# Optimization experiments

Hardware: AMD Instinct MI355X
Metric: run time of the kernel (lower is better)

Reference implementation:

```python
import jax, jax.numpy as jnp
import numpy as np

EPS = 1e-5
NUM_HEADS = 8
KEY_DIM = 16
D = 64  # attn_ratio * key_dim


def conv1x1_bn(x, w, g, b, m, v):
    # x: (B, Cin, H, W), w: (Cout, Cin); eval-mode BatchNorm over channel dim
    y = jnp.einsum('bchw,oc->bohw', x, w)
    scale = (g * jax.lax.rsqrt(v + EPS))[None, :, None, None]
    shift = (b - g * m * jax.lax.rsqrt(v + EPS))[None, :, None, None]
    return y * scale + shift


def setup_inputs() -> dict:
    key = jax.random.key(0)
    ks = jax.random.split(key, 22)
    dim, nh_kd, dh = 384, 128, 512
    f = jax.random.normal
    u = jax.random.uniform
    return {
        'x': f(ks[0], (2, dim, 56, 56), jnp.float32),
        'wq': f(ks[1], (nh_kd, dim), jnp.float32) * 0.05,
        'qg': u(ks[2], (nh_kd,), jnp.float32), 'qb': f(ks[3], (nh_kd,)) * 0.1,
        'qm': f(ks[4], (nh_kd,)) * 0.1, 'qv': u(ks[5], (nh_kd,)) + 0.5,
        'wk': f(ks[6], (nh_kd, dim), jnp.float32) * 0.05,
        'kg': u(ks[7], (nh_kd,), jnp.float32), 'kb': f(ks[8], (nh_kd,)) * 0.1,
        'km': f(ks[9], (nh_kd,)) * 0.1, 'kvv': u(ks[10], (nh_kd,)) + 0.5,
        'wv': f(ks[11], (dh, dim), jnp.float32) * 0.05,
        'vg': u(ks[12], (dh,), jnp.float32), 'vb': f(ks[13], (dh,)) * 0.1,
        'vm': f(ks[14], (dh,)) * 0.1, 'vvv': u(ks[15], (dh,)) + 0.5,
        'wp': f(ks[16], (dim, dh), jnp.float32) * 0.05,
        'pg': u(ks[17], (dim,), jnp.float32), 'pb': f(ks[18], (dim,)) * 0.1,
        'pm': f(ks[19], (dim,)) * 0.1, 'pvv': u(ks[20], (dim,)) + 0.5,
    }


def reference(x, wq, qg, qb, qm, qv, wk, kg, kb, km, kvv,
              wv, vg, vb, vm, vvv, wp, pg, pb, pm, pvv):
    B, C, H, W = x.shape
    N = H * W
    h, kd, d = NUM_HEADS, KEY_DIM, D
    # (B, h, N, kd)
    qq = conv1x1_bn(x, wq, qg, qb, qm, qv).reshape(B, h, kd, N).transpose(0, 1, 3, 2)
    # (B, h, kd, N)
    kk = conv1x1_bn(x, wk, kg, kb, km, kvv).reshape(B, h, kd, N)
    # (B, h, N, d)
    vv = conv1x1_bn(x, wv, vg, vb, vm, vvv).reshape(B, h, d, N).transpose(0, 1, 3, 2)
    # NOTE: original forward does NOT apply self.scale
    attn = jax.nn.softmax(jnp.matmul(qq, kk), axis=-1)  # (B, h, N, N)
    xx = jnp.matmul(attn, vv)                            # (B, h, N, d)
    xx = xx.transpose(0, 1, 3, 2).reshape(B, h * d, H, W)
    xx = jax.nn.relu(xx)
    return conv1x1_bn(xx, wp, pg, pb, pm, pvv)
```

## Files before the change

kernel.cpp:

```cpp
#include <hip/hip_runtime.h>
#include <hip/hip_bf16.h>

#define B_   2
#define CIN  384
#define NPIX 3136
#define NH   8
#define KD   16
#define DHEAD 64
#define NHKD 128
#define DHD  512
#define EPSW 1e-5f

typedef __attribute__((ext_vector_type(8))) short vshort8;
typedef __attribute__((ext_vector_type(4))) short vshort4;
typedef __attribute__((ext_vector_type(4))) float vfloat4;

static __device__ __forceinline__ float bf2f(short s) {
    unsigned int u = ((unsigned int)(unsigned short)s) << 16;
    return __builtin_bit_cast(float, u);
}
static __device__ __forceinline__ short f2bf(float f) {
    unsigned int u = __builtin_bit_cast(unsigned int, f);
    unsigned int lsb = (u >> 16) & 1u;
    u += 0x7fffu + lsb;
    return (short)(u >> 16);
}
static __device__ __forceinline__ float pget(const void* p, int i, int f32) {
    return f32 ? ((const float*)p)[i] : bf2f(((const short*)p)[i]);
}

__global__ void detect_dtype(const unsigned short* __restrict__ x, int* __restrict__ flag) {
    if (threadIdx.x == 0 && blockIdx.x == 0) {
        int big = 0;
        for (int i = 0; i < 512; i += 2) {
            int e = (x[i] >> 7) & 0xFF;
            if (e >= 0xC0) big++;
        }
        *flag = (big >= 8) ? 1 : 0;
    }
}

__global__ __launch_bounds__(256) void convert_weights(
    const void* __restrict__ wq, const void* __restrict__ wk,
    const void* __restrict__ wv, const void* __restrict__ wp,
    short* __restrict__ wB, const int* __restrict__ flag)
{
    int f32 = *flag;
    int i = blockIdx.x * 256 + threadIdx.x;
    const void* src; int j;
    if (i < 49152)       { src = wq; j = i; }
    else if (i < 98304)  { src = wk; j = i - 49152; }
    else if (i < 294912) { src = wv; j = i - 98304; }
    else                 { src = wp; j = i - 294912; }
    wB[i] = f32 ? f2bf(((const float*)src)[j]) : ((const short*)src)[j];
}

__global__ __launch_bounds__(256) void transpose_k(const void* __restrict__ x,
                                                   short* __restrict__ xT,
                                                   const int* __restrict__ flag) {
    __shared__ short tile[32][33];
    int f32 = *flag;
    int b = blockIdx.z, n0 = blockIdx.x * 32, c0 = blockIdx.y * 32;
    int t = threadIdx.x;
    int r = t >> 3, q4 = (t & 7) * 4;
    size_t off = ((size_t)b * CIN + c0 + r) * NPIX + n0 + q4;
    if (f32) {
        float4 v = *(const float4*)((const float*)x + off);
        tile[r][q4 + 0] = f2bf(v.x);
        tile[r][q4 + 1] = f2bf(v.y);
        tile[r][q4 + 2] = f2bf(v.z);
        tile[r][q4 + 3] = f2bf(v.w);
    } else {
        vshort4 v = *(const vshort4*)((const short*)x + off);
#pragma unroll
        for (int i = 0; i < 4; i++) tile[r][q4 + i] = v[i];
    }
    __syncthreads();
    vshort4 o;
#pragma unroll
    for (int i = 0; i < 4; i++) o[i] = tile[q4 + i][r];
    *(vshort4*)(xT + ((size_t)b * NPIX + n0 + r) * CIN + c0 + q4) = o;
}

__global__ __launch_bounds__(256) void gemm_bt_bn(
    const short* __restrict__ A, long sAb,
    const short* __restrict__ Bt, long sBb,
    void* __restrict__ C, long sCb,
    const void* __restrict__ g, const void* __restrict__ bb,
    const void* __restrict__ mn, const void* __restrict__ vr,
    int Ma, int Nb, int K, int bnPerRow, int finalOut,
    const int* __restrict__ flag)
{
    __shared__ __attribute__((aligned(16))) short Al[64 * 72];
    __shared__ __attribute__((aligned(16))) short Bl[64 * 72];
    int f32 = *flag;
    int b = blockIdx.z;
    const short* Ab = A + (size_t)b * sAb;
    const short* Bb = Bt + (size_t)b * sBb;
    size_t cbase = (size_t)b * sCb;
    int m0 = blockIdx.x * 64, n0 = blockIdx.y * 64;
    int t = threadIdx.x, lane = t & 63, w = t >> 6, m = lane & 15, quad = lane >> 4;
    int srow = t >> 2, scol = (t & 3) * 16;
    const short* ag = Ab + (size_t)(m0 + srow) * K + scol;
    const short* bg = Bb + (size_t)(n0 + srow) * K + scol;
    vfloat4 acc[4];
#pragma unroll
    for (int i = 0; i < 4; i++) acc[i] = (vfloat4){0.f, 0.f, 0.f, 0.f};

    for (int k0 = 0; k0 < K; k0 += 64) {
        vshort8 a0 = *(const vshort8*)(ag + k0);
        vshort8 a1 = *(const vshort8*)(ag + k0 + 8);
        vshort8 b0 = *(const vshort8*)(bg + k0);
        vshort8 b1 = *(const vshort8*)(bg + k0 + 8);
        __syncthreads();
        *(vshort8*)&Al[srow * 72 + scol] = a0;
        *(vshort8*)&Al[srow * 72 + scol + 8] = a1;
        *(vshort8*)&Bl[srow * 72 + scol] = b0;
        *(vshort8*)&Bl[srow * 72 + scol + 8] = b1;
        __syncthreads();
#pragma unroll
        for (int kk = 0; kk < 2; kk++) {
            vshort8 af = *(const vshort8*)&Al[(w * 16 + m) * 72 + kk * 32 + quad * 8];
#pragma unroll
            for (int nc = 0; nc < 4; nc++) {
                vshort8 bf = *(const vshort8*)&Bl[(nc * 16 + m) * 72 + kk * 32 + quad * 8];
                acc[nc] = __builtin_amdgcn_mfma_f32_16x16x32_bf16(af, bf, acc[nc], 0, 0, 0);
            }
        }
    }

#pragma unroll
    for (int nc = 0; nc < 4; nc++) {
#pragma unroll
        for (int r = 0; r < 4; r++) {
            int row = m0 + w * 16 + quad * 4 + r;
            int col = n0 + nc * 16 + m;
            int ch = bnPerRow ? row : col;
            float iv = rsqrtf(pget(vr, ch, f32) + EPSW);
            float sc = pget(g, ch, f32) * iv;
            float sh = pget(bb, ch, f32) - pget(mn, ch, f32) * sc;
            float val = sc * acc[nc][r] + sh;
            size_t idx = cbase + (size_t)row * Nb + col;
            if (finalOut && f32) ((float*)C)[idx] = val;
            else                 ((short*)C)[idx] = f2bf(val);
        }
    }
}

__global__ __launch_bounds__(256) void attn_kernel(
    const short* __restrict__ Qt, const short* __restrict__ Kt,
    const short* __restrict__ V, short* __restrict__ xx)
{
    __shared__ __attribute__((aligned(16))) short Kl[64 * 40];
    __shared__ __attribute__((aligned(16))) short Vl[64 * 72];
    __shared__ __attribute__((aligned(16))) short Pl[64 * 72];
    __shared__ float Ls[64];
    int bh = blockIdx.y, b = bh >> 3, h = bh & 7;
    int q0 = blockIdx.x * 64;
    int t = threadIdx.x, lane = t & 63, w = t >> 6, m = lane & 15, quad = lane >> 4;

    {
        int key = t >> 2;
        int z = 16 + (t & 3) * 4;
        *(vshort4*)&Kl[key * 40 + z] = (vshort4){0, 0, 0, 0};
    }

    int q = q0 + w * 16 + m;
    vshort8 aq;
    if (quad < 2) {
        aq = *(const vshort8*)(Qt + ((size_t)b * NPIX + q) * NHKD + h * KD + quad * 8);
    } else {
        aq = (vshort8){0, 0, 0, 0, 0, 0, 0, 0};
    }

    vfloat4 o[4];
#pragma unroll
    for (int i = 0; i < 4; i++) o[i] = (vfloat4){0.f, 0.f, 0.f, 0.f};
    float Lr = 0.f;

    int skey = t >> 2, skd = (t & 3) * 4;
    const short* kgp = Kt + ((size_t)b * NPIX) * NHKD + h * KD + skd;
    int vrow = t >> 2, vcol = (t & 3) * 16;
    const short* vgp = V + ((size_t)(b * DHD) + h * DHEAD + vrow) * NPIX + vcol;
    const vfloat4 zero4 = (vfloat4){0.f, 0.f, 0.f, 0.f};

    for (int k0 = 0; k0 < NPIX; k0 += 64) {
        vshort4 kstg = *(const vshort4*)(kgp + (size_t)(k0 + skey) * NHKD);
        vshort8 v0 = *(const vshort8*)(vgp + k0);
        vshort8 v1 = *(const vshort8*)(vgp + k0 + 8);
        __syncthreads();
        *(vshort4*)&Kl[skey * 40 + skd] = kstg;
        *(vshort8*)&Vl[vrow * 72 + vcol] = v0;
        *(vshort8*)&Vl[vrow * 72 + vcol + 8] = v1;
        __syncthreads();

        vfloat4 s[4];
#pragma unroll
        for (int c = 0; c < 4; c++) {
            vshort8 ak = *(const vshort8*)&Kl[(c * 16 + m) * 40 + quad * 8];
            s[c] = __builtin_amdgcn_mfma_f32_16x16x32_bf16(ak, aq, zero4, 0, 0, 0);
        }

        short* pw = &Pl[(w * 16 + m) * 72];
#pragma unroll
        for (int c = 0; c < 4; c++) {
            vshort4 pv;
#pragma unroll
            for (int r = 0; r < 4; r++) {
                float p = __expf(s[c][r]);
                Lr += p;
                pv[r] = f2bf(p);
            }
            *(vshort4*)&pw[c * 16 + quad * 4] = pv;
        }

#pragma unroll
        for (int kc = 0; kc < 2; kc++) {
            vshort8 ap = *(const vshort8*)&Pl[(w * 16 + m) * 72 + kc * 32 + quad * 8];
#pragma unroll
            for (int dc = 0; dc < 4; dc++) {
                vshort8 bv = *(const vshort8*)&Vl[(dc * 16 + m) * 72 + kc * 32 + quad * 8];
                o[dc] = __builtin_amdgcn_mfma_f32_16x16x32_bf16(ap, bv, o[dc], 0, 0, 0);
            }
        }
    }

    Lr += __shfl_xor(Lr, 16);
    Lr += __shfl_xor(Lr, 32);
    Ls[w * 16 + m] = Lr;
    __syncthreads();

#pragma unroll
    for (int r = 0; r < 4; r++) {
        float inv = 1.0f / Ls[w * 16 + quad * 4 + r];
        int qrow = q0 + w * 16 + quad * 4 + r;
        size_t base = ((size_t)b * NPIX + qrow) * DHD + h * DHEAD + m;
#pragma unroll
        for (int dc = 0; dc < 4; dc++) {
            float val = o[dc][r] * inv;
            val = fmaxf(val, 0.0f);
            xx[base + dc * 16] = f2bf(val);
        }
    }
}

extern "C" void kernel_launch(void* const* d_in, const int* in_sizes, int n_in,
                              void* d_out, int out_size, void* d_ws, size_t ws_size,
                              hipStream_t stream) {
    const void* x  = d_in[0];
    const void* wq = d_in[1];
    const void* qg = d_in[2];  const void* qb = d_in[3];
    const void* qm = d_in[4];  const void* qv = d_in[5];
    const void* wk = d_in[6];
    const void* kg = d_in[7];  const void* kb = d_in[8];
    const void* km = d_in[9];  const void* kv = d_in[10];
    const void* wv = d_in[11];
    const void* vg = d_in[12]; const void* vb = d_in[13];
    const void* vm = d_in[14]; const void* vv = d_in[15];
    const void* wp = d_in[16];
    const void* pg = d_in[17]; const void* pb = d_in[18];
    const void* pm = d_in[19]; const void* pv = d_in[20];

    short* xT  = (short*)d_ws;
    short* wB  = xT + (size_t)B_ * NPIX * CIN;
    short* wqB = wB;
    short* wkB = wB + 49152;
    short* wvB = wB + 98304;
    short* wpB = wB + 294912;
    short* Qt  = wB + 491520;
    short* Kt  = Qt + (size_t)B_ * NPIX * NHKD;
    short* Vb  = Kt + (size_t)B_ * NPIX * NHKD;
    short* xx  = Vb + (size_t)B_ * DHD * NPIX;
    int* flag  = (int*)(xx + (size_t)B_ * NPIX * DHD);

    detect_dtype<<<1, 64, 0, stream>>>((const unsigned short*)x, flag);
    convert_weights<<<491520 / 256, 256, 0, stream>>>(wq, wk, wv, wp, wB, flag);
    transpose_k<<<dim3(NPIX / 32, CIN / 32, B_), 256, 0, stream>>>(x, xT, flag);

    gemm_bt_bn<<<dim3(NPIX / 64, NHKD / 64, B_), 256, 0, stream>>>(
        xT, (long)NPIX * CIN, wqB, 0, Qt, (long)NPIX * NHKD,
        qg, qb, qm, qv, NPIX, NHKD, CIN, 0, 0, flag);
    gemm_bt_bn<<<dim3(NPIX / 64, NHKD / 64, B_), 256, 0, stream>>>(
        xT, (long)NPIX * CIN, wkB, 0, Kt, (long)NPIX * NHKD,
        kg, kb, km, kv, NPIX, NHKD, CIN, 0, 0, flag);
    gemm_bt_bn<<<dim3(DHD / 64, NPIX / 64, B_), 256, 0, stream>>>(
        wvB, 0, xT, (long)NPIX * CIN, Vb, (long)DHD * NPIX,
        vg, vb, vm, vv, DHD, NPIX, CIN, 1, 0, flag);

    attn_kernel<<<dim3(NPIX / 64, B_ * NH), 256, 0, stream>>>(Qt, Kt, Vb, xx);

    gemm_bt_bn<<<dim3(CIN / 64, NPIX / 64, B_), 256, 0, stream>>>(
        wpB, 0, xx, (long)NPIX * DHD, d_out, (long)CIN * NPIX,
        pg, pb, pm, pv, CIN, NPIX, DHD, 1, 1, flag);
}
```

Before: 236.3 us.

## Double-buffer attention loads, fuse Q/K GEMMs, precompute BN affine, MFMA row sums

New measurement: 214.0 us. 1.1x faster.

```diff
diff --git a/kernel.cpp b/kernel.cpp
--- a/kernel.cpp
+++ b/kernel.cpp
@@ -8,6 +8,7 @@
 #define KD   16
 #define DHEAD 64
 #define NHKD 128
+#define QKW  256
 #define DHD  512
 #define EPSW 1e-5f
 
@@ -30,29 +31,54 @@
 }
 
 __global__ void detect_dtype(const unsigned short* __restrict__ x, int* __restrict__ flag) {
-    if (threadIdx.x == 0 && blockIdx.x == 0) {
-        int big = 0;
-        for (int i = 0; i < 512; i += 2) {
-            int e = (x[i] >> 7) & 0xFF;
-            if (e >= 0xC0) big++;
-        }
-        *flag = (big >= 8) ? 1 : 0;
-    }
-}
-
-__global__ __launch_bounds__(256) void convert_weights(
+    int lane = threadIdx.x & 63;
+    int cnt = 0;
+#pragma unroll
+    for (int j = 0; j < 8; j++) {
+        int e = (x[(lane * 8 + j) * 2] >> 7) & 0xFF;
+        cnt += (e >= 0xC0);
+    }
+    cnt += __shfl_xor(cnt, 1);
+    cnt += __shfl_xor(cnt, 2);
+    cnt += __shfl_xor(cnt, 4);
+    cnt += __shfl_xor(cnt, 8);
+    cnt += __shfl_xor(cnt, 16);
+    cnt += __shfl_xor(cnt, 32);
+    if (threadIdx.x == 0) *flag = (cnt >= 16) ? 1 : 0;
+}
+
+__global__ __launch_bounds__(256) void convert_and_bn(
     const void* __restrict__ wq, const void* __restrict__ wk,
     const void* __restrict__ wv, const void* __restrict__ wp,
-    short* __restrict__ wB, const int* __restrict__ flag)
+    short* __restrict__ wB,
+    const void* qg, const void* qb, const void* qm, const void* qv,
+    const void* kg, const void* kb, const void* km, const void* kv,
+    const void* vg, const void* vb, const void* vm, const void* vv,
+    const void* pg, const void* pb, const void* pm, const void* pv,
+    float* __restrict__ scA, float* __restrict__ shA,
+    const int* __restrict__ flag)
 {
     int f32 = *flag;
     int i = blockIdx.x * 256 + threadIdx.x;
-    const void* src; int j;
-    if (i < 49152)       { src = wq; j = i; }
-    else if (i < 98304)  { src = wk; j = i - 49152; }
-    else if (i < 294912) { src = wv; j = i - 98304; }
-    else                 { src = wp; j = i - 294912; }
-    wB[i] = f32 ? f2bf(((const float*)src)[j]) : ((const short*)src)[j];
+    {
+        const void* src; int j;
+        if (i < 49152)       { src = wq; j = i; }
+        else if (i < 98304)  { src = wk; j = i - 49152; }
+        else if (i < 294912) { src = wv; j = i - 98304; }
+        else                 { src = wp; j = i - 294912; }
+        wB[i] = f32 ? f2bf(((const float*)src)[j]) : ((const short*)src)[j];
+    }
+    if (i < 1152) {
+        const void *g, *bb, *mn, *vr; int j;
+        if (i < 128)      { g = qg; bb = qb; mn = qm; vr = qv; j = i; }
+        else if (i < 256) { g = kg; bb = kb; mn = km; vr = kv; j = i - 128; }
+        else if (i < 768) { g = vg; bb = vb; mn = vm; vr = vv; j = i - 256; }
+        else              { g = pg; bb = pb; mn = pm; vr = pv; j = i - 768; }
+        float iv = rsqrtf(pget(vr, j, f32) + EPSW);
+        float s = pget(g, j, f32) * iv;
+        scA[i] = s;
+        shA[i] = pget(bb, j, f32) - pget(mn, j, f32) * s;
+    }
 }
 
 __global__ __launch_bounds__(256) void transpose_k(const void* __restrict__ x,
@@ -86,14 +112,13 @@
     const short* __restrict__ A, long sAb,
     const short* __restrict__ Bt, long sBb,
     void* __restrict__ C, long sCb,
-    const void* __restrict__ g, const void* __restrict__ bb,
-    const void* __restrict__ mn, const void* __restrict__ vr,
-    int Ma, int Nb, int K, int bnPerRow, int finalOut,
+    const float* __restrict__ sc, const float* __restrict__ sh,
+    int Nb, int K, int bnPerRow, int finalOut,
     const int* __restrict__ flag)
 {
     __shared__ __attribute__((aligned(16))) short Al[64 * 72];
     __shared__ __attribute__((aligned(16))) short Bl[64 * 72];
-    int f32 = *flag;
+    int f32 = finalOut ? *flag : 0;
     int b = blockIdx.z;
     const short* Ab = A + (size_t)b * sAb;
     const short* Bb = Bt + (size_t)b * sBb;
@@ -131,15 +156,15 @@
 
 #pragma unroll
     for (int nc = 0; nc < 4; nc++) {
+        int col = n0 + nc * 16 + m;
+        float scc = bnPerRow ? 0.f : sc[col];
+        float shc = bnPerRow ? 0.f : sh[col];
 #pragma unroll
         for (int r = 0; r < 4; r++) {
             int row = m0 + w * 16 + quad * 4 + r;
-            int col = n0 + nc * 16 + m;
-            int ch = bnPerRow ? row : col;
-            float iv = rsqrtf(pget(vr, ch, f32) + EPSW);
-            float sc = pget(g, ch, f32) * iv;
-            float sh = pget(bb, ch, f32) - pget(mn, ch, f32) * sc;
-            float val = sc * acc[nc][r] + sh;
+            float s2 = bnPerRow ? sc[row] : scc;
+            float h2 = bnPerRow ? sh[row] : shc;
+            float val = s2 * acc[nc][r] + h2;
             size_t idx = cbase + (size_t)row * Nb + col;
             if (finalOut && f32) ((float*)C)[idx] = val;
             else                 ((short*)C)[idx] = f2bf(val);
@@ -148,13 +173,12 @@
 }
 
 __global__ __launch_bounds__(256) void attn_kernel(
-    const short* __restrict__ Qt, const short* __restrict__ Kt,
-    const short* __restrict__ V, short* __restrict__ xx)
+    const short* __restrict__ QKt, const short* __restrict__ V,
+    short* __restrict__ xx)
 {
-    __shared__ __attribute__((aligned(16))) short Kl[64 * 40];
-    __shared__ __attribute__((aligned(16))) short Vl[64 * 72];
+    __shared__ __attribute__((aligned(16))) short Kl[2][64 * 40];
+    __shared__ __attribute__((aligned(16))) short Vl[2][64 * 72];
     __shared__ __attribute__((aligned(16))) short Pl[64 * 72];
-    __shared__ float Ls[64];
     int bh = blockIdx.y, b = bh >> 3, h = bh & 7;
     int q0 = blockIdx.x * 64;
     int t = threadIdx.x, lane = t & 63, w = t >> 6, m = lane & 15, quad = lane >> 4;
@@ -162,42 +186,56 @@
     {
         int key = t >> 2;
         int z = 16 + (t & 3) * 4;
-        *(vshort4*)&Kl[key * 40 + z] = (vshort4){0, 0, 0, 0};
+        *(vshort4*)&Kl[0][key * 40 + z] = (vshort4){0, 0, 0, 0};
+        *(vshort4*)&Kl[1][key * 40 + z] = (vshort4){0, 0, 0, 0};
     }
 
     int q = q0 + w * 16 + m;
     vshort8 aq;
     if (quad < 2) {
-        aq = *(const vshort8*)(Qt + ((size_t)b * NPIX + q) * NHKD + h * KD + quad * 8);
+        aq = *(const vshort8*)(QKt + ((size_t)b * NPIX + q) * QKW + h * KD + quad * 8);
     } else {
         aq = (vshort8){0, 0, 0, 0, 0, 0, 0, 0};
     }
 
-    vfloat4 o[4];
+    vfloat4 o[4], o4;
 #pragma unroll
     for (int i = 0; i < 4; i++) o[i] = (vfloat4){0.f, 0.f, 0.f, 0.f};
-    float Lr = 0.f;
+    o4 = (vfloat4){0.f, 0.f, 0.f, 0.f};
 
     int skey = t >> 2, skd = (t & 3) * 4;
-    const short* kgp = Kt + ((size_t)b * NPIX) * NHKD + h * KD + skd;
+    const short* kgp = QKt + (size_t)b * NPIX * QKW + NHKD + h * KD + skd;
     int vrow = t >> 2, vcol = (t & 3) * 16;
     const short* vgp = V + ((size_t)(b * DHD) + h * DHEAD + vrow) * NPIX + vcol;
     const vfloat4 zero4 = (vfloat4){0.f, 0.f, 0.f, 0.f};
-
-    for (int k0 = 0; k0 < NPIX; k0 += 64) {
-        vshort4 kstg = *(const vshort4*)(kgp + (size_t)(k0 + skey) * NHKD);
-        vshort8 v0 = *(const vshort8*)(vgp + k0);
-        vshort8 v1 = *(const vshort8*)(vgp + k0 + 8);
-        __syncthreads();
-        *(vshort4*)&Kl[skey * 40 + skd] = kstg;
-        *(vshort8*)&Vl[vrow * 72 + vcol] = v0;
-        *(vshort8*)&Vl[vrow * 72 + vcol + 8] = v1;
-        __syncthreads();
+    const short one_bf = (short)0x3F80;
+    const vshort8 ones = {one_bf, one_bf, one_bf, one_bf, one_bf, one_bf, one_bf, one_bf};
+
+    {
+        vshort4 kstg = *(const vshort4*)(kgp + (size_t)skey * QKW);
+        vshort8 v0 = *(const vshort8*)(vgp);
+        vshort8 v1 = *(const vshort8*)(vgp + 8);
+        *(vshort4*)&Kl[0][skey * 40 + skd] = kstg;
+        *(vshort8*)&Vl[0][vrow * 72 + vcol] = v0;
+        *(vshort8*)&Vl[0][vrow * 72 + vcol + 8] = v1;
+    }
+    __syncthreads();
+
+    for (int it = 0; it < NPIX / 64; ++it) {
+        int cur = it & 1, nxt = cur ^ 1;
+        int k0 = it * 64;
+        int more = (it + 1) < (NPIX / 64);
+        vshort4 kstg; vshort8 v0, v1;
+        if (more) {
+            kstg = *(const vshort4*)(kgp + (size_t)(k0 + 64 + skey) * QKW);
+            v0 = *(const vshort8*)(vgp + k0 + 64);
+            v1 = *(const vshort8*)(vgp + k0 + 72);
+        }
 
         vfloat4 s[4];
 #pragma unroll
         for (int c = 0; c < 4; c++) {
-            vshort8 ak = *(const vshort8*)&Kl[(c * 16 + m) * 40 + quad * 8];
+            vshort8 ak = *(const vshort8*)&Kl[cur][(c * 16 + m) * 40 + quad * 8];
             s[c] = __builtin_amdgcn_mfma_f32_16x16x32_bf16(ak, aq, zero4, 0, 0, 0);
         }
 
@@ -208,8 +246,7 @@
 #pragma unroll
             for (int r = 0; r < 4; r++) {
                 float p = __expf(s[c][r]);
-                Lr += p;
-                pv[r] = f2bf(p);
+                pv[r] = (short)(__builtin_bit_cast(unsigned int, p) >> 16);
             }
             *(vshort4*)&pw[c * 16 + quad * 4] = pv;
         }
@@ -219,20 +256,23 @@
             vshort8 ap = *(const vshort8*)&Pl[(w * 16 + m) * 72 + kc * 32 + quad * 8];
 #pragma unroll
             for (int dc = 0; dc < 4; dc++) {
-                vshort8 bv = *(const vshort8*)&Vl[(dc * 16 + m) * 72 + kc * 32 + quad * 8];
+                vshort8 bv = *(const vshort8*)&Vl[cur][(dc * 16 + m) * 72 + kc * 32 + quad * 8];
                 o[dc] = __builtin_amdgcn_mfma_f32_16x16x32_bf16(ap, bv, o[dc], 0, 0, 0);
             }
-        }
-    }
-
-    Lr += __shfl_xor(Lr, 16);
-    Lr += __shfl_xor(Lr, 32);
-    Ls[w * 16 + m] = Lr;
-    __syncthreads();
+            o4 = __builtin_amdgcn_mfma_f32_16x16x32_bf16(ap, ones, o4, 0, 0, 0);
+        }
+
+        if (more) {
+            *(vshort4*)&Kl[nxt][skey * 40 + skd] = kstg;
+            *(vshort8*)&Vl[nxt][vrow * 72 + vcol] = v0;
+            *(vshort8*)&Vl[nxt][vrow * 72 + vcol + 8] = v1;
+        }
+        __syncthreads();
+    }
 
 #pragma unroll
     for (int r = 0; r < 4; r++) {
-        float inv = 1.0f / Ls[w * 16 + quad * 4 + r];
+        float inv = 1.0f / o4[r];
         int qrow = q0 + w * 16 + quad * 4 + r;
         size_t base = ((size_t)b * NPIX + qrow) * DHD + h * DHEAD + m;
 #pragma unroll
@@ -263,33 +303,33 @@
 
     short* xT  = (short*)d_ws;
     short* wB  = xT + (size_t)B_ * NPIX * CIN;
-    short* wqB = wB;
-    short* wkB = wB + 49152;
-    short* wvB = wB + 98304;
-    short* wpB = wB + 294912;
-    short* Qt  = wB + 491520;
-    short* Kt  = Qt + (size_t)B_ * NPIX * NHKD;
-    short* Vb  = Kt + (size_t)B_ * NPIX * NHKD;
+    short* wqkB = wB;
+    short* wvB  = wB + 98304;
+    short* wpB  = wB + 294912;
+    short* QKt = wB + 491520;
+    short* Vb  = QKt + (size_t)B_ * NPIX * QKW;
     short* xx  = Vb + (size_t)B_ * DHD * NPIX;
-    int* flag  = (int*)(xx + (size_t)B_ * NPIX * DHD);
+    float* scA = (float*)(xx + (size_t)B_ * NPIX * DHD);
+    float* shA = scA + 1152;
+    int* flag  = (int*)(shA + 1152);
 
     detect_dtype<<<1, 64, 0, stream>>>((const unsigned short*)x, flag);
-    convert_weights<<<491520 / 256, 256, 0, stream>>>(wq, wk, wv, wp, wB, flag);
+    convert_and_bn<<<491520 / 256, 256, 0, stream>>>(
+        wq, wk, wv, wp, wB,
+        qg, qb, qm, qv, kg, kb, km, kv,
+        vg, vb, vm, vv, pg, pb, pm, pv, scA, shA, flag);
     transpose_k<<<dim3(NPIX / 32, CIN / 32, B_), 256, 0, stream>>>(x, xT, flag);
 
-    gemm_bt_bn<<<dim3(NPIX / 64, NHKD / 64, B_), 256, 0, stream>>>(
-        xT, (long)NPIX * CIN, wqB, 0, Qt, (long)NPIX * NHKD,
-        qg, qb, qm, qv, NPIX, NHKD, CIN, 0, 0, flag);
-    gemm_bt_bn<<<dim3(NPIX / 64, NHKD / 64, B_), 256, 0, stream>>>(
-        xT, (long)NPIX * CIN, wkB, 0, Kt, (long)NPIX * NHKD,
-        kg, kb, km, kv, NPIX, NHKD, CIN, 0, 0, flag);
+    gemm_bt_bn<<<dim3(NPIX / 64, QKW / 64, B_), 256, 0, stream>>>(
+        xT, (long)NPIX * CIN, wqkB, 0, QKt, (long)NPIX * QKW,
+        scA, shA, QKW, CIN, 0, 0, flag);
     gemm_bt_bn<<<dim3(DHD / 64, NPIX / 64, B_), 256, 0, stream>>>(
         wvB, 0, xT, (long)NPIX * CIN, Vb, (long)DHD * NPIX,
-        vg, vb, vm, vv, DHD, NPIX, CIN, 1, 0, flag);
-
-    attn_kernel<<<dim3(NPIX / 64, B_ * NH), 256, 0, stream>>>(Qt, Kt, Vb, xx);
+        scA + 256, shA + 256, NPIX, CIN, 1, 0, flag);
+
+    attn_kernel<<<dim3(NPIX / 64, B_ * NH), 256, 0, stream>>>(QKt, Vb, xx);
 
     gemm_bt_bn<<<dim3(CIN / 64, NPIX / 64, B_), 256, 0, stream>>>(
         wpB, 0, xx, (long)NPIX * DHD, d_out, (long)CIN * NPIX,
-        pg, pb, pm, pv, CIN, NPIX, DHD, 1, 1, flag);
-}
+        scA + 768, shA + 768, NPIX, DHD, 1, 1, flag);
+}
```
